# Kernel tuning notes

Measured on AMD Instinct MI355X. Metric: run time of the kernel, lower is better.

## Reference

```python
import jax, jax.numpy as jnp
import numpy as np

N = 20000   # nodes
D = 128     # fiber_dim
H = 8       # heads
P = 8       # point_dim = D // (H*2)
E = 320000  # edges
L = 4       # n_stacks
EPS = 1e-4


def _w(k, shape):
    fan_in = shape[-2] if len(shape) >= 2 else shape[-1]
    return jax.random.normal(k, shape, dtype=jnp.float32) / np.sqrt(fan_in)


def setup_inputs() -> dict:
    key = jax.random.key(0)
    ks = jax.random.split(key, 24)
    x = jax.random.normal(ks[0], (N, 4, D), dtype=jnp.float32)
    t = jax.random.normal(ks[1], (N, D), dtype=jnp.float32)
    Rm, _ = jnp.linalg.qr(jax.random.normal(ks[2], (N, 3, 3), dtype=jnp.float32))  # proper frames
    x_edge = jax.random.normal(ks[3], (E, D), dtype=jnp.float32)
    edge_index = jax.random.randint(ks[4], (2, E), 0, N)
    dh = D // H
    return {
        'x': x, 't': t, 'R': Rm, 'x_edge': x_edge, 'edge_index': edge_index,
        'Wq': _w(ks[5], (L, 2 * D, D)), 'Wk': _w(ks[6], (L, 2 * D, D)), 'Wv': _w(ks[7], (L, 2 * D, D)),
        'Wpq': _w(ks[8], (L, D, H * P)), 'Wpk': _w(ks[9], (L, D, H * P)), 'Wpv': _w(ks[10], (L, D, H * P)),
        'We': _w(ks[11], (L, D, H)), 'gamma': jax.random.normal(ks[12], (L, H), dtype=jnp.float32),
        'Wos': _w(ks[13], (L, D + H * P, D)), 'Wov': _w(ks[14], (L, H * P, D)),
        'We1': _w(ks[15], (L, 3 * D, D)), 'We2': _w(ks[16], (L, D, D)),
        'luW1': _w(ks[17], (L, 5 * D, 5 * D)), 'lub1': jnp.zeros((L, 5 * D), jnp.float32),
        'luW2': _w(ks[18], (L, 5 * D, 4 * D)) * 0.1, 'lub2': jnp.zeros((L, 4 * D), jnp.float32),
    }


def _forward(x, t, R, x_edge, edge_index, Wq, Wk, Wv, Wpq, Wpk, Wpv, We, gamma,
             Wos, Wov, We1, We2, luW1, lub1, luW2, lub2):
    src, dst = edge_index[0], edge_index[1]
    dh = D // H
    for l in range(L):
        s, v = x[:, 0], x[:, 1:]                      # [N,D], [N,3,D]
        st = jnp.concatenate([s, t], axis=-1)          # [N,2D] scalar feats + time enc
        q = (st @ Wq[l]).reshape(-1, H, dh)
        k = (st @ Wk[l]).reshape(-1, H, dh)
        val = (st @ Wv[l]).reshape(-1, H, dh)
        pq = jnp.einsum('nic,cp->nip', v, Wpq[l]).reshape(-1, 3, H, P)
        pk = jnp.einsum('nic,cp->nip', v, Wpk[l]).reshape(-1, 3, H, P)
        pv = jnp.einsum('nic,cp->nip', v, Wpv[l]).reshape(-1, 3, H, P)
        dots = jnp.einsum('ehd,ehd->eh', q[dst], k[src]) / np.sqrt(dh)
        dp = pq[dst] - pk[src]                         # [E,3,H,P]
        dist = jnp.sum(dp * dp, axis=(1, 3))           # [E,H]
        logits = dots + x_edge @ We[l] - jax.nn.softplus(gamma[l]) * dist
        m = jax.ops.segment_max(logits, dst, num_segments=N)
        w = jnp.exp(logits - m[dst])
        denom = jax.ops.segment_sum(w, dst, num_segments=N)
        alpha = w / denom[dst]                         # [E,H] softmax over incoming edges
        out_s = jax.ops.segment_sum(alpha[:, :, None] * val[src], dst, num_segments=N).reshape(-1, D)
        out_p = jax.ops.segment_sum(alpha[:, None, :, None] * pv[src], dst, num_segments=N)  # [N,3,H,P]
        pn = jnp.sqrt(jnp.sum(out_p * out_p, axis=1) + EPS).reshape(-1, H * P)
        s_out = jnp.concatenate([out_s, pn], axis=-1) @ Wos[l]
        v_out = jnp.einsum('nip,pc->nic', out_p.reshape(-1, 3, H * P), Wov[l])
        x = x + jnp.concatenate([s_out[:, None], v_out], axis=1)
        e_in = jnp.concatenate([s[src], s[dst], x_edge], axis=-1)
        x_edge = x_edge + jax.nn.gelu(e_in @ We1[l], approximate=False) @ We2[l]
        # LocalUpdateUsingReferenceRotations
        s2, v2 = x[:, 0], x[:, 1:]
        vloc = jnp.einsum('nic,nij->ncj', v2, R).reshape(-1, 3 * D)  # rotate to local frame
        vn = jnp.sqrt(jnp.sum(v2 * v2, axis=1) + EPS)
        z = jnp.concatenate([s2, vloc, vn], axis=-1)   # [N,5D]
        h = (jax.nn.gelu(z @ luW1[l] + lub1[l], approximate=False) @ luW2[l] + lub2[l]).reshape(-1, 4, D)
        vglob = jnp.einsum('nij,njc->nic', R, h[:, 1:])
        x = x + jnp.concatenate([h[:, :1], vglob], axis=1)
    return x, x_edge


def reference(x, t, R, x_edge, edge_index, Wq, Wk, Wv, Wpq, Wpk, Wpv, We, gamma,
              Wos, Wov, We1, We2, luW1, lub1, luW2, lub2):
    return _forward(x, t, R, x_edge, edge_index, Wq, Wk, Wv, Wpq, Wpk, Wpv, We,
                    gamma, Wos, Wov, We1, We2, luW1, lub1, luW2, lub2)
```

## Files before the change

### kernel.cpp

```cpp
#include <hip/hip_runtime.h>
#include <math.h>

#define NN 20000
#define DD 128
#define HH 8
#define PP 8
#define EE 320000
#define LL 4
#define EPSF 1e-4f

__global__ void count_kernel(const int* __restrict__ dst, int* __restrict__ counts) {
    int e = blockIdx.x * 256 + threadIdx.x;
    if (e < EE) atomicAdd(&counts[dst[e]], 1);
}

__global__ void scan_kernel(const int* __restrict__ counts, int* __restrict__ offs) {
    __shared__ int tmp[1024];
    __shared__ int carry;
    if (threadIdx.x == 0) { carry = 0; offs[0] = 0; }
    __syncthreads();
    for (int base = 0; base < NN; base += 1024) {
        int i = base + threadIdx.x;
        int v = (i < NN) ? counts[i] : 0;
        tmp[threadIdx.x] = v;
        __syncthreads();
        for (int off = 1; off < 1024; off <<= 1) {
            int add = (threadIdx.x >= off) ? tmp[threadIdx.x - off] : 0;
            __syncthreads();
            tmp[threadIdx.x] += add;
            __syncthreads();
        }
        if (i < NN) offs[i + 1] = carry + tmp[threadIdx.x];
        __syncthreads();
        if (threadIdx.x == 0) carry += tmp[1023];
        __syncthreads();
    }
}

__global__ void fill_kernel(const int* __restrict__ dst, const int* __restrict__ offs,
                            int* __restrict__ cursor, int* __restrict__ perm) {
    int e = blockIdx.x * 256 + threadIdx.x;
    if (e < EE) {
        int d = dst[e];
        int p = atomicAdd(&cursor[d], 1);
        perm[offs[d] + p] = e;
    }
}

__global__ void proj_kernel(const float* __restrict__ x, const float* __restrict__ t,
                            const float* __restrict__ Wq, const float* __restrict__ Wk,
                            const float* __restrict__ Wv,
                            const float* __restrict__ Wpq, const float* __restrict__ Wpk,
                            const float* __restrict__ Wpv,
                            float* __restrict__ s_old,
                            float* __restrict__ q, float* __restrict__ k, float* __restrict__ val,
                            float* __restrict__ pq, float* __restrict__ pk, float* __restrict__ pv) {
    __shared__ float lds[8 * 384];
    int n0 = blockIdx.x * 8;
    int tid = threadIdx.x;
    for (int idx = tid; idx < 8 * 256; idx += 256) {
        int node = idx >> 8, c = idx & 255;
        int n = n0 + node;
        float vv = 0.f;
        if (n < NN) vv = (c < 128) ? x[(size_t)n * 512 + c] : t[(size_t)n * 128 + (c - 128)];
        lds[node * 256 + c] = vv;
        if (n < NN && c < 128) s_old[(size_t)n * 128 + c] = vv;
    }
    __syncthreads();
    {
        int col = tid & 127;
        int half = tid >> 7;
        float aq[4] = {0, 0, 0, 0}, ak[4] = {0, 0, 0, 0}, av[4] = {0, 0, 0, 0};
        for (int kk = 0; kk < 256; kk++) {
            float wq = Wq[kk * 128 + col], wk = Wk[kk * 128 + col], wv = Wv[kk * 128 + col];
#pragma unroll
            for (int r = 0; r < 4; r++) {
                float a = lds[(half * 4 + r) * 256 + kk];
                aq[r] += a * wq; ak[r] += a * wk; av[r] += a * wv;
            }
        }
        for (int r = 0; r < 4; r++) {
            int n = n0 + half * 4 + r;
            if (n < NN) {
                q[(size_t)n * 128 + col] = aq[r];
                k[(size_t)n * 128 + col] = ak[r];
                val[(size_t)n * 128 + col] = av[r];
            }
        }
    }
    __syncthreads();
    for (int idx = tid; idx < 8 * 384; idx += 256) {
        int node = idx / 384, c = idx % 384;
        int n = n0 + node;
        lds[node * 384 + c] = (n < NN) ? x[(size_t)n * 512 + 128 + c] : 0.f;
    }
    __syncthreads();
    {
        int hp = tid & 63;
        int grp = tid >> 6;
        float apq[3][2], apk[3][2], apv[3][2];
        for (int i = 0; i < 3; i++) for (int r = 0; r < 2; r++) { apq[i][r] = 0; apk[i][r] = 0; apv[i][r] = 0; }
        for (int c = 0; c < 128; c++) {
            float wq = Wpq[c * 64 + hp], wk = Wpk[c * 64 + hp], wv = Wpv[c * 64 + hp];
#pragma unroll
            for (int i = 0; i < 3; i++)
#pragma unroll
                for (int r = 0; r < 2; r++) {
                    float a = lds[(grp * 2 + r) * 384 + i * 128 + c];
                    apq[i][r] += a * wq; apk[i][r] += a * wk; apv[i][r] += a * wv;
                }
        }
        for (int r = 0; r < 2; r++) {
            int n = n0 + grp * 2 + r;
            if (n < NN)
                for (int i = 0; i < 3; i++) {
                    pq[(size_t)n * 192 + i * 64 + hp] = apq[i][r];
                    pk[(size_t)n * 192 + i * 64 + hp] = apk[i][r];
                    pv[(size_t)n * 192 + i * 64 + hp] = apv[i][r];
                }
        }
    }
}

__global__ void logits_kernel(const int* __restrict__ src, const int* __restrict__ dst,
                              const float* __restrict__ q, const float* __restrict__ k,
                              const float* __restrict__ pq, const float* __restrict__ pk,
                              const float* __restrict__ xe, const float* __restrict__ We_l,
                              const float* __restrict__ gamma_l,
                              float* __restrict__ logits) {
    int tid = threadIdx.x;
    int e = blockIdx.x * 32 + (tid >> 3);
    int h = tid & 7;
    if (e >= EE) return;
    int se = src[e], de = dst[e];
    const float* qd = q + (size_t)de * 128 + h * 16;
    const float* ks = k + (size_t)se * 128 + h * 16;
    float dot = 0.f;
#pragma unroll
    for (int d = 0; d < 16; d++) dot += qd[d] * ks[d];
    float dist = 0.f;
    const float* pqd = pq + (size_t)de * 192 + h * 8;
    const float* pks = pk + (size_t)se * 192 + h * 8;
#pragma unroll
    for (int i = 0; i < 3; i++)
#pragma unroll
        for (int p = 0; p < 8; p++) {
            float dpp = pqd[i * 64 + p] - pks[i * 64 + p];
            dist += dpp * dpp;
        }
    float bias = 0.f;
    const float* xer = xe + (size_t)e * 128;
    for (int c = 0; c < 128; c++) bias += xer[c] * We_l[c * 8 + h];
    float g = gamma_l[h];
    float sp = log1pf(expf(g));
    logits[(size_t)e * 8 + h] = dot * 0.25f + bias - sp * dist;
}

__global__ void agg_kernel(const int* __restrict__ offs, const int* __restrict__ perm,
                           const int* __restrict__ src, const float* __restrict__ logits,
                           const float* __restrict__ val, const float* __restrict__ pv,
                           float* __restrict__ out_s, float* __restrict__ out_p) {
    int wid = threadIdx.x >> 6;
    int lane = threadIdx.x & 63;
    int n = blockIdx.x * 4 + wid;
    if (n >= NN) return;
    int base = offs[n];
    int deg = offs[n + 1] - base;
    float m = -1e30f, ssum = 0.f;
    if (lane < 8) {
        for (int j = 0; j < deg; j++) {
            int e = perm[base + j];
            float lg = logits[(size_t)e * 8 + lane];
            float mn = fmaxf(m, lg);
            ssum = ssum * __expf(m - mn) + __expf(lg - mn);
            m = mn;
        }
    }
    int hA = lane >> 4;
    int hB = hA + 4;
    int hC = lane >> 3;
    float mA = __shfl(m, hA), dA = __shfl(ssum, hA);
    float mB = __shfl(m, hB), dB = __shfl(ssum, hB);
    float mC = __shfl(m, hC), dC = __shfl(ssum, hC);
    float rA = (dA > 0.f) ? 1.f / dA : 0.f;
    float rB = (dB > 0.f) ? 1.f / dB : 0.f;
    float rC = (dC > 0.f) ? 1.f / dC : 0.f;
    float accs0 = 0, accs1 = 0, accp0 = 0, accp1 = 0, accp2 = 0;
    for (int j = 0; j < deg; j++) {
        int e = perm[base + j];
        int s_ = src[e];
        float aA = __expf(logits[(size_t)e * 8 + hA] - mA) * rA;
        float aB = __expf(logits[(size_t)e * 8 + hB] - mB) * rB;
        float aC = __expf(logits[(size_t)e * 8 + hC] - mC) * rC;
        accs0 += aA * val[(size_t)s_ * 128 + lane];
        accs1 += aB * val[(size_t)s_ * 128 + 64 + lane];
        accp0 += aC * pv[(size_t)s_ * 192 + lane];
        accp1 += aC * pv[(size_t)s_ * 192 + 64 + lane];
        accp2 += aC * pv[(size_t)s_ * 192 + 128 + lane];
    }
    out_s[(size_t)n * 128 + lane] = accs0;
    out_s[(size_t)n * 128 + 64 + lane] = accs1;
    out_p[(size_t)n * 192 + lane] = accp0;
    out_p[(size_t)n * 192 + 64 + lane] = accp1;
    out_p[(size_t)n * 192 + 128 + lane] = accp2;
}

__global__ void attn_out_kernel(const float* __restrict__ out_s, const float* __restrict__ out_p,
                                const float* __restrict__ Wos_l, const float* __restrict__ Wov_l,
                                float* __restrict__ x) {
    __shared__ float lds[8 * 384];
    int n0 = blockIdx.x * 8;
    int tid = threadIdx.x;
    for (int idx = tid; idx < 8 * 128; idx += 256) {
        int node = idx >> 7, c = idx & 127;
        int n = n0 + node;
        lds[node * 384 + c] = (n < NN) ? out_s[(size_t)n * 128 + c] : 0.f;
    }
    for (int idx = tid; idx < 8 * 192; idx += 256) {
        int node = idx / 192, c = idx % 192;
        int n = n0 + node;
        lds[node * 384 + 192 + c] = (n < NN) ? out_p[(size_t)n * 192 + c] : 0.f;
    }
    __syncthreads();
    for (int idx = tid; idx < 8 * 64; idx += 256) {
        int node = idx >> 6, hp = idx & 63;
        float* b = lds + node * 384;
        float p0 = b[192 + hp], p1 = b[192 + 64 + hp], p2 = b[192 + 128 + hp];
        b[128 + hp] = sqrtf(p0 * p0 + p1 * p1 + p2 * p2 + EPSF);
    }
    __syncthreads();
    int col = tid & 127;
    int grp = tid >> 7;
    float as[4] = {0, 0, 0, 0}, av0[4] = {0, 0, 0, 0}, av1[4] = {0, 0, 0, 0}, av2[4] = {0, 0, 0, 0};
    for (int kk = 0; kk < 192; kk++) {
        float w = Wos_l[kk * 128 + col];
#pragma unroll
        for (int r = 0; r < 4; r++) as[r] += lds[(grp * 4 + r) * 384 + kk] * w;
    }
    for (int p = 0; p < 64; p++) {
        float w = Wov_l[p * 128 + col];
#pragma unroll
        for (int r = 0; r < 4; r++) {
            float* b = lds + (grp * 4 + r) * 384 + 192;
            av0[r] += b[p] * w; av1[r] += b[64 + p] * w; av2[r] += b[128 + p] * w;
        }
    }
    for (int r = 0; r < 4; r++) {
        int n = n0 + grp * 4 + r;
        if (n < NN) {
            x[(size_t)n * 512 + col] += as[r];
            x[(size_t)n * 512 + 128 + col] += av0[r];
            x[(size_t)n * 512 + 256 + col] += av1[r];
            x[(size_t)n * 512 + 384 + col] += av2[r];
        }
    }
}

__global__ __launch_bounds__(256) void edge_mlp_kernel(const int* __restrict__ src,
                                                       const int* __restrict__ dst,
                                                       const float* __restrict__ Y1,
                                                       const float* __restrict__ Y2,
                                                       const float* __restrict__ We1c,
                                                       const float* __restrict__ We2_l,
                                                       float* __restrict__ xe) {
    __shared__ float As[16][65];
    __shared__ float Bs[16][132];
    __shared__ float Hs[64][132];
    int e0 = blockIdx.x * 64;
    int tid = threadIdx.x;
    int ty = tid >> 4, tx = tid & 15;
    float acc[4][8];
#pragma unroll
    for (int r = 0; r < 4; r++) {
        int e = e0 + ty * 4 + r;
        const float* y1 = Y1 + (size_t)src[e] * 128;
        const float* y2 = Y2 + (size_t)dst[e] * 128;
        float4 u0 = *(const float4*)(y1 + tx * 4);
        float4 v0 = *(const float4*)(y2 + tx * 4);
        float4 u1 = *(const float4*)(y1 + 64 + tx * 4);
        float4 v1 = *(const float4*)(y2 + 64 + tx * 4);
        acc[r][0] = u0.x + v0.x; acc[r][1] = u0.y + v0.y;
        acc[r][2] = u0.z + v0.z; acc[r][3] = u0.w + v0.w;
        acc[r][4] = u1.x + v1.x; acc[r][5] = u1.y + v1.y;
        acc[r][6] = u1.z + v1.z; acc[r][7] = u1.w + v1.w;
    }
    for (int kt = 0; kt < 8; kt++) {
        int kbase = kt * 16;
        {
            int m = tid >> 2, kq = (tid & 3) * 4;
            float4 v = *(const float4*)(xe + (size_t)(e0 + m) * 128 + kbase + kq);
            As[kq + 0][m] = v.x; As[kq + 1][m] = v.y; As[kq + 2][m] = v.z; As[kq + 3][m] = v.w;
        }
#pragma unroll
        for (int i = 0; i < 2; i++) {
            int idx4 = tid * 2 + i;
            int rr = idx4 >> 5, cc = (idx4 & 31) * 4;
            float4 v = *(const float4*)(We1c + (size_t)(kbase + rr) * 128 + cc);
            Bs[rr][cc] = v.x; Bs[rr][cc + 1] = v.y; Bs[rr][cc + 2] = v.z; Bs[rr][cc + 3] = v.w;
        }
        __syncthreads();
#pragma unroll
        for (int kk = 0; kk < 16; kk++) {
            float a[4], b[8];
#pragma unroll
            for (int r = 0; r < 4; r++) a[r] = As[kk][ty * 4 + r];
#pragma unroll
            for (int c = 0; c < 4; c++) { b[c] = Bs[kk][tx * 4 + c]; b[4 + c] = Bs[kk][64 + tx * 4 + c]; }
#pragma unroll
            for (int r = 0; r < 4; r++)
#pragma unroll
                for (int c = 0; c < 8; c++) acc[r][c] += a[r] * b[c];
        }
        __syncthreads();
    }
#pragma unroll
    for (int r = 0; r < 4; r++)
#pragma unroll
        for (int c = 0; c < 4; c++) {
            float v = acc[r][c];
            Hs[ty * 4 + r][tx * 4 + c] = 0.5f * v * (1.f + erff(v * 0.70710678118f));
            float w = acc[r][4 + c];
            Hs[ty * 4 + r][64 + tx * 4 + c] = 0.5f * w * (1.f + erff(w * 0.70710678118f));
        }
    __syncthreads();
#pragma unroll
    for (int r = 0; r < 4; r++)
#pragma unroll
        for (int c = 0; c < 8; c++) acc[r][c] = 0.f;
    for (int kt = 0; kt < 8; kt++) {
        int kbase = kt * 16;
#pragma unroll
        for (int i = 0; i < 2; i++) {
            int idx4 = tid * 2 + i;
            int rr = idx4 >> 5, cc = (idx4 & 31) * 4;
            float4 v = *(const float4*)(We2_l + (size_t)(kbase + rr) * 128 + cc);
            Bs[rr][cc] = v.x; Bs[rr][cc + 1] = v.y; Bs[rr][cc + 2] = v.z; Bs[rr][cc + 3] = v.w;
        }
        __syncthreads();
#pragma unroll
        for (int kk = 0; kk < 16; kk++) {
            float a[4], b[8];
#pragma unroll
            for (int r = 0; r < 4; r++) a[r] = Hs[ty * 4 + r][kbase + kk];
#pragma unroll
            for (int c = 0; c < 4; c++) { b[c] = Bs[kk][tx * 4 + c]; b[4 + c] = Bs[kk][64 + tx * 4 + c]; }
#pragma unroll
            for (int r = 0; r < 4; r++)
#pragma unroll
                for (int c = 0; c < 8; c++) acc[r][c] += a[r] * b[c];
        }
        __syncthreads();
    }
#pragma unroll
    for (int r = 0; r < 4; r++) {
        float* row = xe + (size_t)(e0 + ty * 4 + r) * 128;
        float4 o0 = *(const float4*)(row + tx * 4);
        float4 o1 = *(const float4*)(row + 64 + tx * 4);
        o0.x += acc[r][0]; o0.y += acc[r][1]; o0.z += acc[r][2]; o0.w += acc[r][3];
        o1.x += acc[r][4]; o1.y += acc[r][5]; o1.z += acc[r][6]; o1.w += acc[r][7];
        *(float4*)(row + tx * 4) = o0;
        *(float4*)(row + 64 + tx * 4) = o1;
    }
}

__global__ void zprep_kernel(const float* __restrict__ x, const float* __restrict__ R,
                             float* __restrict__ z) {
    int idx = blockIdx.x * 256 + threadIdx.x;
    if (idx >= NN * 128) return;
    int n = idx >> 7, c = idx & 127;
    float v0 = x[(size_t)n * 512 + 128 + c];
    float v1 = x[(size_t)n * 512 + 256 + c];
    float v2 = x[(size_t)n * 512 + 384 + c];
    const float* Rn = R + (size_t)n * 9;
    float* zr = z + (size_t)n * 640;
    zr[c] = x[(size_t)n * 512 + c];
    zr[128 + c * 3 + 0] = v0 * Rn[0] + v1 * Rn[3] + v2 * Rn[6];
    zr[128 + c * 3 + 1] = v0 * Rn[1] + v1 * Rn[4] + v2 * Rn[7];
    zr[128 + c * 3 + 2] = v0 * Rn[2] + v1 * Rn[5] + v2 * Rn[8];
    zr[512 + c] = sqrtf(v0 * v0 + v1 * v1 + v2 * v2 + EPSF);
}

template <int ACT>
__global__ __launch_bounds__(256) void gemm_bias_kernel(const float* __restrict__ A,
                                                        const float* __restrict__ B,
                                                        const float* __restrict__ bias,
                                                        float* __restrict__ C,
                                                        int M, int K, int Nc) {
    __shared__ float As[16][65];
    __shared__ float Bs[16][132];
    int m0 = blockIdx.x * 64;
    int n0_ = blockIdx.y * 128;
    int tid = threadIdx.x;
    int ty = tid >> 4, tx = tid & 15;
    float acc[4][8];
#pragma unroll
    for (int r = 0; r < 4; r++)
#pragma unroll
        for (int c = 0; c < 8; c++) acc[r][c] = 0.f;
    for (int kt = 0; kt < K; kt += 16) {
        {
            int m = tid >> 2, kq = (tid & 3) * 4;
            int gm = m0 + m;
            float4 v = make_float4(0.f, 0.f, 0.f, 0.f);
            if (gm < M) v = *(const float4*)(A + (size_t)gm * K + kt + kq);
            As[kq + 0][m] = v.x; As[kq + 1][m] = v.y; As[kq + 2][m] = v.z; As[kq + 3][m] = v.w;
        }
#pragma unroll
        for (int i = 0; i < 2; i++) {
            int idx4 = tid * 2 + i;
            int rr = idx4 >> 5, cc = (idx4 & 31) * 4;
            float4 v = *(const float4*)(B + (size_t)(kt + rr) * Nc + n0_ + cc);
            Bs[rr][cc] = v.x; Bs[rr][cc + 1] = v.y; Bs[rr][cc + 2] = v.z; Bs[rr][cc + 3] = v.w;
        }
        __syncthreads();
#pragma unroll
        for (int kk = 0; kk < 16; kk++) {
            float a[4], b[8];
#pragma unroll
            for (int r = 0; r < 4; r++) a[r] = As[kk][ty * 4 + r];
#pragma unroll
            for (int c = 0; c < 4; c++) { b[c] = Bs[kk][tx * 4 + c]; b[4 + c] = Bs[kk][64 + tx * 4 + c]; }
#pragma unroll
            for (int r = 0; r < 4; r++)
#pragma unroll
                for (int c = 0; c < 8; c++) acc[r][c] += a[r] * b[c];
        }
        __syncthreads();
    }
#pragma unroll
    for (int r = 0; r < 4; r++) {
        int gm = m0 + ty * 4 + r;
        if (gm < M) {
#pragma unroll
            for (int c = 0; c < 4; c++) {
                int gc0 = n0_ + tx * 4 + c;
                int gc1 = n0_ + 64 + tx * 4 + c;
                float v = acc[r][c] + (bias ? bias[gc0] : 0.f);
                float w = acc[r][4 + c] + (bias ? bias[gc1] : 0.f);
                if (ACT) {
                    v = 0.5f * v * (1.f + erff(v * 0.70710678118f));
                    w = 0.5f * w * (1.f + erff(w * 0.70710678118f));
                }
                C[(size_t)gm * Nc + gc0] = v;
                C[(size_t)gm * Nc + gc1] = w;
            }
        }
    }
}

__global__ void final_kernel(const float* __restrict__ h, const float* __restrict__ R,
                             float* __restrict__ x) {
    int idx = blockIdx.x * 256 + threadIdx.x;
    if (idx >= NN * 128) return;
    int n = idx >> 7, c = idx & 127;
    const float* hr = h + (size_t)n * 512;
    const float* Rn = R + (size_t)n * 9;
    float h1 = hr[128 + c], h2 = hr[256 + c], h3 = hr[384 + c];
    x[(size_t)n * 512 + c] += hr[c];
    x[(size_t)n * 512 + 128 + c] += Rn[0] * h1 + Rn[1] * h2 + Rn[2] * h3;
    x[(size_t)n * 512 + 256 + c] += Rn[3] * h1 + Rn[4] * h2 + Rn[5] * h3;
    x[(size_t)n * 512 + 384 + c] += Rn[6] * h1 + Rn[7] * h2 + Rn[8] * h3;
}

extern "C" void kernel_launch(void* const* d_in, const int* in_sizes, int n_in,
                              void* d_out, int out_size, void* d_ws, size_t ws_size,
                              hipStream_t stream) {
    const float* x_in = (const float*)d_in[0];
    const float* t    = (const float*)d_in[1];
    const float* R    = (const float*)d_in[2];
    const float* xe_in = (const float*)d_in[3];
    const int* ei     = (const int*)d_in[4];
    const float* Wq   = (const float*)d_in[5];
    const float* Wk   = (const float*)d_in[6];
    const float* Wv   = (const float*)d_in[7];
    const float* Wpq  = (const float*)d_in[8];
    const float* Wpk  = (const float*)d_in[9];
    const float* Wpv  = (const float*)d_in[10];
    const float* We   = (const float*)d_in[11];
    const float* gamma = (const float*)d_in[12];
    const float* Wos  = (const float*)d_in[13];
    const float* Wov  = (const float*)d_in[14];
    const float* We1  = (const float*)d_in[15];
    const float* We2  = (const float*)d_in[16];
    const float* luW1 = (const float*)d_in[17];
    const float* lub1 = (const float*)d_in[18];
    const float* luW2 = (const float*)d_in[19];
    const float* lub2 = (const float*)d_in[20];

    float* x  = (float*)d_out;
    float* xe = (float*)d_out + (size_t)NN * 512;

    float* fws = (float*)d_ws;
    float* s_old = fws;                     fws += (size_t)NN * 128;
    float* U = fws;                         fws += (size_t)NN * 1792;
    float* logits = fws;                    fws += (size_t)EE * 8;
    int* iws = (int*)fws;
    int* counts = iws;                      iws += NN + 1;
    int* offs = iws;                        iws += NN + 1;
    int* cursor = iws;                      iws += NN + 1;
    int* perm = iws;                        iws += EE;

    float* q  = U;
    float* k  = U + (size_t)NN * 128;
    float* vv = U + (size_t)NN * 256;
    float* pq = U + (size_t)NN * 384;
    float* pk = U + (size_t)NN * 576;
    float* pv = U + (size_t)NN * 768;
    float* out_s = U + (size_t)NN * 960;
    float* out_p = U + (size_t)NN * 1088;
    float* Y1 = U + (size_t)NN * 1280;
    float* Y2 = U + (size_t)NN * 1408;
    float* z  = U;
    float* h1 = U + (size_t)NN * 640;
    float* h  = U + (size_t)NN * 1280;

    const int* srcp = ei;
    const int* dstp = ei + EE;

    hipMemcpyAsync(x, x_in, (size_t)NN * 512 * 4, hipMemcpyDeviceToDevice, stream);
    hipMemcpyAsync(xe, xe_in, (size_t)EE * 128 * 4, hipMemcpyDeviceToDevice, stream);
    hipMemsetAsync(counts, 0, (NN + 1) * 4, stream);
    hipMemsetAsync(cursor, 0, (NN + 1) * 4, stream);
    count_kernel<<<(EE + 255) / 256, 256, 0, stream>>>(dstp, counts);
    scan_kernel<<<1, 1024, 0, stream>>>(counts, offs);
    fill_kernel<<<(EE + 255) / 256, 256, 0, stream>>>(dstp, offs, cursor, perm);

    for (int l = 0; l < LL; l++) {
        const float* Wq_l = Wq + (size_t)l * 256 * 128;
        const float* Wk_l = Wk + (size_t)l * 256 * 128;
        const float* Wv_l = Wv + (size_t)l * 256 * 128;
        const float* Wpq_l = Wpq + (size_t)l * 128 * 64;
        const float* Wpk_l = Wpk + (size_t)l * 128 * 64;
        const float* Wpv_l = Wpv + (size_t)l * 128 * 64;
        const float* We_l = We + (size_t)l * 128 * 8;
        const float* gamma_l = gamma + (size_t)l * 8;
        const float* Wos_l = Wos + (size_t)l * 192 * 128;
        const float* Wov_l = Wov + (size_t)l * 64 * 128;
        const float* We1_l = We1 + (size_t)l * 384 * 128;
        const float* We2_l = We2 + (size_t)l * 128 * 128;
        const float* luW1_l = luW1 + (size_t)l * 640 * 640;
        const float* lub1_l = lub1 + (size_t)l * 640;
        const float* luW2_l = luW2 + (size_t)l * 640 * 512;
        const float* lub2_l = lub2 + (size_t)l * 512;

        proj_kernel<<<(NN + 7) / 8, 256, 0, stream>>>(x, t, Wq_l, Wk_l, Wv_l, Wpq_l, Wpk_l,
                                                      Wpv_l, s_old, q, k, vv, pq, pk, pv);
        gemm_bias_kernel<0><<<dim3((NN + 63) / 64, 1), 256, 0, stream>>>(
            s_old, We1_l, nullptr, Y1, NN, 128, 128);
        gemm_bias_kernel<0><<<dim3((NN + 63) / 64, 1), 256, 0, stream>>>(
            s_old, We1_l + 128 * 128, nullptr, Y2, NN, 128, 128);
        logits_kernel<<<EE / 32, 256, 0, stream>>>(srcp, dstp, q, k, pq, pk, xe, We_l, gamma_l,
                                                   logits);
        agg_kernel<<<NN / 4, 256, 0, stream>>>(offs, perm, srcp, logits, vv, pv, out_s, out_p);
        attn_out_kernel<<<(NN + 7) / 8, 256, 0, stream>>>(out_s, out_p, Wos_l, Wov_l, x);
        edge_mlp_kernel<<<EE / 64, 256, 0, stream>>>(srcp, dstp, Y1, Y2, We1_l + 256 * 128,
                                                     We2_l, xe);
        zprep_kernel<<<(NN * 128 + 255) / 256, 256, 0, stream>>>(x, R, z);
        gemm_bias_kernel<1><<<dim3((NN + 63) / 64, 5), 256, 0, stream>>>(z, luW1_l, lub1_l, h1,
                                                                         NN, 640, 640);
        gemm_bias_kernel<0><<<dim3((NN + 63) / 64, 4), 256, 0, stream>>>(h1, luW2_l, lub2_l, h,
                                                                         NN, 640, 512);
        final_kernel<<<(NN * 128 + 255) / 256, 256, 0, stream>>>(h, R, x);
    }
}
```

Measured before the change: 5.955 ms.

## Prefetch GEMM tiles into registers, parallelize softmax stats across lanes, pad Hs

The shared GEMM kernel and the edge MLP kernel now load the next K-tile of A and B into registers while the current tile is being computed, giving software double-buffering over global loads. The B tiles are stored and read from shared memory as float4, and the Hs buffer gets padding to reduce bank conflicts. In the aggregation kernel, the online-softmax max and sum are now computed by all 64 lanes, each taking a strided subset of edges, and merged with xor shuffles instead of running on 8 serial lanes. The edge index and src gather for the next edge is also fetched one step ahead. These changes raise register pressure somewhat.

New measurement: 5.763 ms. -3.2%, faster.

```diff
diff --git a/kernel.cpp b/kernel.cpp
--- a/kernel.cpp
+++ b/kernel.cpp
@@ -167,12 +167,21 @@
     int base = offs[n];
     int deg = offs[n + 1] - base;
     float m = -1e30f, ssum = 0.f;
-    if (lane < 8) {
-        for (int j = 0; j < deg; j++) {
+    {
+        int h = lane & 7, js = lane >> 3;
+        for (int j = js; j < deg; j += 8) {
             int e = perm[base + j];
-            float lg = logits[(size_t)e * 8 + lane];
+            float lg = logits[(size_t)e * 8 + h];
             float mn = fmaxf(m, lg);
             ssum = ssum * __expf(m - mn) + __expf(lg - mn);
+            m = mn;
+        }
+#pragma unroll
+        for (int off = 8; off < 64; off <<= 1) {
+            float mo = __shfl_xor(m, off);
+            float so = __shfl_xor(ssum, off);
+            float mn = fmaxf(m, mo);
+            ssum = ssum * __expf(m - mn) + so * __expf(mo - mn);
             m = mn;
         }
     }
@@ -186,9 +195,11 @@
     float rB = (dB > 0.f) ? 1.f / dB : 0.f;
     float rC = (dC > 0.f) ? 1.f / dC : 0.f;
     float accs0 = 0, accs1 = 0, accp0 = 0, accp1 = 0, accp2 = 0;
+    int ecur = 0, scur = 0;
+    if (deg > 0) { ecur = perm[base]; scur = src[ecur]; }
     for (int j = 0; j < deg; j++) {
-        int e = perm[base + j];
-        int s_ = src[e];
+        int e = ecur, s_ = scur;
+        if (j + 1 < deg) { ecur = perm[base + j + 1]; scur = src[ecur]; }
         float aA = __expf(logits[(size_t)e * 8 + hA] - mA) * rA;
         float aB = __expf(logits[(size_t)e * 8 + hB] - mB) * rB;
         float aC = __expf(logits[(size_t)e * 8 + hC] - mC) * rC;
@@ -265,10 +276,12 @@
                                                        float* __restrict__ xe) {
     __shared__ float As[16][65];
     __shared__ float Bs[16][132];
-    __shared__ float Hs[64][132];
+    __shared__ float Hs[64][133];
     int e0 = blockIdx.x * 64;
     int tid = threadIdx.x;
     int ty = tid >> 4, tx = tid & 15;
+    int am = tid >> 2, akq = (tid & 3) * 4;
+    int brr = (tid * 2) >> 5, bcc = ((tid * 2) & 31) * 4;
     float acc[4][8];
 #pragma unroll
     for (int r = 0; r < 4; r++) {
@@ -284,28 +297,32 @@
         acc[r][4] = u1.x + v1.x; acc[r][5] = u1.y + v1.y;
         acc[r][6] = u1.z + v1.z; acc[r][7] = u1.w + v1.w;
     }
+    float4 pa, pb0, pb1;
+    pa  = *(const float4*)(xe + (size_t)(e0 + am) * 128 + akq);
+    pb0 = *(const float4*)(We1c + (size_t)brr * 128 + bcc);
+    pb1 = *(const float4*)(We1c + (size_t)brr * 128 + bcc + 4);
     for (int kt = 0; kt < 8; kt++) {
-        int kbase = kt * 16;
-        {
-            int m = tid >> 2, kq = (tid & 3) * 4;
-            float4 v = *(const float4*)(xe + (size_t)(e0 + m) * 128 + kbase + kq);
-            As[kq + 0][m] = v.x; As[kq + 1][m] = v.y; As[kq + 2][m] = v.z; As[kq + 3][m] = v.w;
-        }
-#pragma unroll
-        for (int i = 0; i < 2; i++) {
-            int idx4 = tid * 2 + i;
-            int rr = idx4 >> 5, cc = (idx4 & 31) * 4;
-            float4 v = *(const float4*)(We1c + (size_t)(kbase + rr) * 128 + cc);
-            Bs[rr][cc] = v.x; Bs[rr][cc + 1] = v.y; Bs[rr][cc + 2] = v.z; Bs[rr][cc + 3] = v.w;
-        }
-        __syncthreads();
+        As[akq + 0][am] = pa.x; As[akq + 1][am] = pa.y;
+        As[akq + 2][am] = pa.z; As[akq + 3][am] = pa.w;
+        *(float4*)&Bs[brr][bcc] = pb0;
+        *(float4*)&Bs[brr][bcc + 4] = pb1;
+        __syncthreads();
+        if (kt < 7) {
+            int kb = (kt + 1) * 16;
+            pa  = *(const float4*)(xe + (size_t)(e0 + am) * 128 + kb + akq);
+            pb0 = *(const float4*)(We1c + (size_t)(kb + brr) * 128 + bcc);
+            pb1 = *(const float4*)(We1c + (size_t)(kb + brr) * 128 + bcc + 4);
+        } else {
+            pb0 = *(const float4*)(We2_l + (size_t)brr * 128 + bcc);
+            pb1 = *(const float4*)(We2_l + (size_t)brr * 128 + bcc + 4);
+        }
 #pragma unroll
         for (int kk = 0; kk < 16; kk++) {
             float a[4], b[8];
 #pragma unroll
             for (int r = 0; r < 4; r++) a[r] = As[kk][ty * 4 + r];
-#pragma unroll
-            for (int c = 0; c < 4; c++) { b[c] = Bs[kk][tx * 4 + c]; b[4 + c] = Bs[kk][64 + tx * 4 + c]; }
+            *(float4*)(b + 0) = *(const float4*)&Bs[kk][tx * 4];
+            *(float4*)(b + 4) = *(const float4*)&Bs[kk][64 + tx * 4];
 #pragma unroll
             for (int r = 0; r < 4; r++)
 #pragma unroll
@@ -322,28 +339,28 @@
             float w = acc[r][4 + c];
             Hs[ty * 4 + r][64 + tx * 4 + c] = 0.5f * w * (1.f + erff(w * 0.70710678118f));
         }
-    __syncthreads();
 #pragma unroll
     for (int r = 0; r < 4; r++)
 #pragma unroll
         for (int c = 0; c < 8; c++) acc[r][c] = 0.f;
+    __syncthreads();
     for (int kt = 0; kt < 8; kt++) {
         int kbase = kt * 16;
-#pragma unroll
-        for (int i = 0; i < 2; i++) {
-            int idx4 = tid * 2 + i;
-            int rr = idx4 >> 5, cc = (idx4 & 31) * 4;
-            float4 v = *(const float4*)(We2_l + (size_t)(kbase + rr) * 128 + cc);
-            Bs[rr][cc] = v.x; Bs[rr][cc + 1] = v.y; Bs[rr][cc + 2] = v.z; Bs[rr][cc + 3] = v.w;
-        }
-        __syncthreads();
+        *(float4*)&Bs[brr][bcc] = pb0;
+        *(float4*)&Bs[brr][bcc + 4] = pb1;
+        __syncthreads();
+        if (kt < 7) {
+            int kb = (kt + 1) * 16;
+            pb0 = *(const float4*)(We2_l + (size_t)(kb + brr) * 128 + bcc);
+            pb1 = *(const float4*)(We2_l + (size_t)(kb + brr) * 128 + bcc + 4);
+        }
 #pragma unroll
         for (int kk = 0; kk < 16; kk++) {
             float a[4], b[8];
 #pragma unroll
             for (int r = 0; r < 4; r++) a[r] = Hs[ty * 4 + r][kbase + kk];
-#pragma unroll
-            for (int c = 0; c < 4; c++) { b[c] = Bs[kk][tx * 4 + c]; b[4 + c] = Bs[kk][64 + tx * 4 + c]; }
+            *(float4*)(b + 0) = *(const float4*)&Bs[kk][tx * 4];
+            *(float4*)(b + 4) = *(const float4*)&Bs[kk][64 + tx * 4];
 #pragma unroll
             for (int r = 0; r < 4; r++)
 #pragma unroll
@@ -392,34 +409,37 @@
     int n0_ = blockIdx.y * 128;
     int tid = threadIdx.x;
     int ty = tid >> 4, tx = tid & 15;
+    int am = tid >> 2, akq = (tid & 3) * 4;
+    int gm = m0 + am;
+    int brr = (tid * 2) >> 5, bcc = ((tid * 2) & 31) * 4;
     float acc[4][8];
 #pragma unroll
     for (int r = 0; r < 4; r++)
 #pragma unroll
         for (int c = 0; c < 8; c++) acc[r][c] = 0.f;
+    float4 pa = make_float4(0.f, 0.f, 0.f, 0.f), pb0, pb1;
+    if (gm < M) pa = *(const float4*)(A + (size_t)gm * K + akq);
+    pb0 = *(const float4*)(B + (size_t)brr * Nc + n0_ + bcc);
+    pb1 = *(const float4*)(B + (size_t)brr * Nc + n0_ + bcc + 4);
     for (int kt = 0; kt < K; kt += 16) {
-        {
-            int m = tid >> 2, kq = (tid & 3) * 4;
-            int gm = m0 + m;
-            float4 v = make_float4(0.f, 0.f, 0.f, 0.f);
-            if (gm < M) v = *(const float4*)(A + (size_t)gm * K + kt + kq);
-            As[kq + 0][m] = v.x; As[kq + 1][m] = v.y; As[kq + 2][m] = v.z; As[kq + 3][m] = v.w;
-        }
-#pragma unroll
-        for (int i = 0; i < 2; i++) {
-            int idx4 = tid * 2 + i;
-            int rr = idx4 >> 5, cc = (idx4 & 31) * 4;
-            float4 v = *(const float4*)(B + (size_t)(kt + rr) * Nc + n0_ + cc);
-            Bs[rr][cc] = v.x; Bs[rr][cc + 1] = v.y; Bs[rr][cc + 2] = v.z; Bs[rr][cc + 3] = v.w;
-        }
-        __syncthreads();
+        As[akq + 0][am] = pa.x; As[akq + 1][am] = pa.y;
+        As[akq + 2][am] = pa.z; As[akq + 3][am] = pa.w;
+        *(float4*)&Bs[brr][bcc] = pb0;
+        *(float4*)&Bs[brr][bcc + 4] = pb1;
+        __syncthreads();
+        if (kt + 16 < K) {
+            pa = make_float4(0.f, 0.f, 0.f, 0.f);
+            if (gm < M) pa = *(const float4*)(A + (size_t)gm * K + kt + 16 + akq);
+            pb0 = *(const float4*)(B + (size_t)(kt + 16 + brr) * Nc + n0_ + bcc);
+            pb1 = *(const float4*)(B + (size_t)(kt + 16 + brr) * Nc + n0_ + bcc + 4);
+        }
 #pragma unroll
         for (int kk = 0; kk < 16; kk++) {
             float a[4], b[8];
 #pragma unroll
             for (int r = 0; r < 4; r++) a[r] = As[kk][ty * 4 + r];
-#pragma unroll
-            for (int c = 0; c < 4; c++) { b[c] = Bs[kk][tx * 4 + c]; b[4 + c] = Bs[kk][64 + tx * 4 + c]; }
+            *(float4*)(b + 0) = *(const float4*)&Bs[kk][tx * 4];
+            *(float4*)(b + 4) = *(const float4*)&Bs[kk][64 + tx * 4];
 #pragma unroll
             for (int r = 0; r < 4; r++)
 #pragma unroll
@@ -429,8 +449,8 @@
     }
 #pragma unroll
     for (int r = 0; r < 4; r++) {
-        int gm = m0 + ty * 4 + r;
-        if (gm < M) {
+        int gm2 = m0 + ty * 4 + r;
+        if (gm2 < M) {
 #pragma unroll
             for (int c = 0; c < 4; c++) {
                 int gc0 = n0_ + tx * 4 + c;
@@ -441,8 +461,8 @@
                     v = 0.5f * v * (1.f + erff(v * 0.70710678118f));
                     w = 0.5f * w * (1.f + erff(w * 0.70710678118f));
                 }
-                C[(size_t)gm * Nc + gc0] = v;
-                C[(size_t)gm * Nc + gc1] = w;
+                C[(size_t)gm2 * Nc + gc0] = v;
+                C[(size_t)gm2 * Nc + gc1] = w;
             }
         }
     }
```
